# Kernel optimization log

Measured on AMD Instinct MI355X. Metric: run time of the kernel, lower is better.

The kernel has to match this reference:

```python
import jax, jax.numpy as jnp
import numpy as np

B, N, D = 8, 9856, 256
HEADS = 8
WH, WW = 7, 11
HID = 512  # int(D * 2.0)
EPS = 1e-5


def layernorm(x, g, b):
    mu = jnp.mean(x, axis=-1, keepdims=True)
    var = jnp.mean(jnp.square(x - mu), axis=-1, keepdims=True)
    return (x - mu) * jax.lax.rsqrt(var + EPS) * g + b


def setup_inputs() -> dict:
    key = jax.random.key(0)
    ks = jax.random.split(key, 6)
    s = lambda k, shape: (jax.random.normal(k, shape, jnp.float32) * 0.02)
    return {
        "x": jax.random.normal(ks[0], (B, N, D), jnp.float32),
        "norm1_g": jnp.ones((D,), jnp.float32),
        "norm1_b": jnp.zeros((D,), jnp.float32),
        "in_proj_w": s(ks[1], (3 * D, D)),
        "in_proj_b": jnp.zeros((3 * D,), jnp.float32),
        "out_w": s(ks[2], (D, D)),
        "out_b": jnp.zeros((D,), jnp.float32),
        "norm2_g": jnp.ones((D,), jnp.float32),
        "norm2_b": jnp.zeros((D,), jnp.float32),
        "fc1_w": s(ks[3], (HID, D)),
        "fc1_b": jnp.zeros((HID,), jnp.float32),
        "fc2_w": s(ks[4], (D, HID)),
        "fc2_b": jnp.zeros((D,), jnp.float32),
        "h": 56,
        "w": 176,
    }


def reference(x, norm1_g, norm1_b, in_proj_w, in_proj_b, out_w, out_b,
              norm2_g, norm2_b, fc1_w, fc1_b, fc2_w, fc2_b, h, w):
    Bx, Nx, Dx = x.shape
    n_h, n_w = h // WH, w // WW  # chosen dims divide evenly -> pad_h = pad_w = 0
    hd = Dx // HEADS
    L = WH * WW  # 77 tokens per window

    res = x
    xn = layernorm(x, norm1_g, norm1_b)

    # window partition: (B, h*w, D) -> (B*n_h*n_w, wh*ww, D)
    win = xn.reshape(Bx, n_h, WH, n_w, WW, Dx)
    win = win.transpose(0, 1, 3, 2, 4, 5).reshape(-1, L, Dx)

    # MultiheadAttention (batch_first) on each window independently
    qkv = win @ in_proj_w.T + in_proj_b          # (NW, L, 3D)
    q, k, v = jnp.split(qkv, 3, axis=-1)
    NW = win.shape[0]
    q = q.reshape(NW, L, HEADS, hd).transpose(0, 2, 1, 3)
    k = k.reshape(NW, L, HEADS, hd).transpose(0, 2, 1, 3)
    v = v.reshape(NW, L, HEADS, hd).transpose(0, 2, 1, 3)
    scores = jnp.einsum("nhld,nhmd->nhlm", q, k) / jnp.sqrt(jnp.float32(hd))
    attn = jax.nn.softmax(scores, axis=-1)
    o = jnp.einsum("nhlm,nhmd->nhld", attn, v)   # (NW, H, L, hd)
    o = o.transpose(0, 2, 1, 3).reshape(NW, L, Dx)
    o = o @ out_w.T + out_b

    # window reverse: (B*n_h*n_w, wh*ww, D) -> (B, h*w, D)
    o = o.reshape(Bx, n_h, n_w, WH, WW, Dx)
    o = o.transpose(0, 1, 3, 2, 4, 5).reshape(Bx, Nx, Dx)

    x = res + o
    res = x
    xn2 = layernorm(x, norm2_g, norm2_b)
    hmid = jax.nn.gelu(xn2 @ fc1_w.T + fc1_b, approximate=False)
    mlp = hmid @ fc2_w.T + fc2_b
    return res + mlp
```

## Files before the change

### kernel.cpp

```cpp
#include <hip/hip_runtime.h>
#include <hip/hip_bf16.h>

typedef unsigned short u16;
typedef unsigned int   u32;

typedef __bf16 bf16x8 __attribute__((ext_vector_type(8)));
typedef float  f32x4  __attribute__((ext_vector_type(4)));

__device__ __forceinline__ u16 f2bf(float f) {
  u32 u = __float_as_uint(f);
  u += 0x7fffu + ((u >> 16) & 1u);
  return (u16)(u >> 16);
}
__device__ __forceinline__ u32 pack2(float a, float b) {
  return (u32)f2bf(a) | ((u32)f2bf(b) << 16);
}
__device__ __forceinline__ void gld16(const void* g, void* l) {
  __builtin_amdgcn_global_load_lds(
      (const __attribute__((address_space(1))) unsigned int*)g,
      (__attribute__((address_space(3))) unsigned int*)l, 16, 0, 0);
}

#define TOK_M   78848
#define DIM     256
#define NWIN    1024
#define WINL    77

__global__ __launch_bounds__(256)
void cvt_w(const float* __restrict__ w0, const float* __restrict__ w1,
           const float* __restrict__ w2, const float* __restrict__ w3,
           u16* __restrict__ out)
{
  const int i = (blockIdx.x * 256 + threadIdx.x) * 4;
  const float* src; int off;
  if      (i < 196608) { src = w0; off = i; }
  else if (i < 262144) { src = w1; off = i - 196608; }
  else if (i < 393216) { src = w2; off = i - 262144; }
  else                 { src = w3; off = i - 393216; }
  float4 v = *(const float4*)(src + off);
  uint2 o; o.x = pack2(v.x, v.y); o.y = pack2(v.z, v.w);
  *(uint2*)(out + i) = o;
}

template<bool PERM>
__global__ __launch_bounds__(256)
void ln_k(const float* __restrict__ X, const float* __restrict__ g,
          const float* __restrict__ bta, u16* __restrict__ Y)
{
  const int tid  = threadIdx.x;
  const int tok  = blockIdx.x * 4 + (tid >> 6);
  const int lane = tid & 63;
  float4 v = *(const float4*)(X + (size_t)tok * DIM + lane * 4);
  float s = v.x + v.y + v.z + v.w;
#pragma unroll
  for (int off = 32; off; off >>= 1) s += __shfl_xor(s, off);
  const float mu = s * (1.f / 256.f);
  const float dx = v.x - mu, dy = v.y - mu, dz = v.z - mu, dw = v.w - mu;
  float q = dx * dx + dy * dy + dz * dz + dw * dw;
#pragma unroll
  for (int off = 32; off; off >>= 1) q += __shfl_xor(q, off);
  const float rstd = rsqrtf(q * (1.f / 256.f) + 1e-5f);
  float4 gg = *(const float4*)(g + lane * 4);
  float4 bb = *(const float4*)(bta + lane * 4);
  const float y0 = dx * rstd * gg.x + bb.x;
  const float y1 = dy * rstd * gg.y + bb.y;
  const float y2 = dz * rstd * gg.z + bb.z;
  const float y3 = dw * rstd * gg.w + bb.w;
  size_t dest = (size_t)tok;
  if (PERM) {
    const int b  = tok / 9856, n = tok - b * 9856;
    const int y  = n / 176,  xc = n - y * 176;
    const int ih = y / 7,    rr = y - ih * 7;
    const int iw = xc / 11,  cc = xc - iw * 11;
    dest = (size_t)(((b * 8 + ih) * 16 + iw)) * 77 + rr * 11 + cc;
  }
  uint2 o;
  o.x = pack2(y0, y1);
  o.y = pack2(y2, y3);
  *(uint2*)(Y + dest * DIM + lane * 4) = o;
}

template<int EPI, int OBF>
__global__ __launch_bounds__(256, 3)
void gemm_mfma(const u16* __restrict__ A, const u16* __restrict__ W,
               const float* __restrict__ bias, const float* res,
               void* Cout, int N, int K)
{
  __shared__ u16 As[4096];
  __shared__ u16 Bs[4096];

  const int tid  = threadIdx.x;
  const int wave = tid >> 6, lane = tid & 63;
  const int wy = wave >> 1, wx = wave & 1;
  const int quad = lane >> 4, l16 = lane & 15;
  const int m0 = blockIdx.x * 128;
  const int n0 = blockIdx.y * 128;

  const int s0 = tid, s1 = tid + 256;
  const int r0 = s0 >> 2, r1 = s1 >> 2;
  const int kb0 = (s0 & 3) ^ (r0 & 3);
  const int kb1 = (s1 & 3) ^ (r1 & 3);
  const u16* Ag0 = A + (size_t)(m0 + r0) * K + kb0 * 8;
  const u16* Ag1 = A + (size_t)(m0 + r1) * K + kb1 * 8;
  const u16* Bg0 = W + (size_t)(n0 + r0) * K + kb0 * 8;
  const u16* Bg1 = W + (size_t)(n0 + r1) * K + kb1 * 8;

  const int kbs = quad ^ (l16 & 3);
  const u16* Ar = &As[(wy * 64 + l16) * 32 + kbs * 8];
  const u16* Br = &Bs[(wx * 64 + l16) * 32 + kbs * 8];

  f32x4 acc[4][4];
#pragma unroll
  for (int i = 0; i < 4; ++i)
#pragma unroll
    for (int j = 0; j < 4; ++j) {
      f32x4 z = {0.f, 0.f, 0.f, 0.f};
      acc[i][j] = z;
    }

  for (int kt = 0; kt < K; kt += 32) {
    gld16(Ag0 + kt, &As[s0 * 8]);
    gld16(Ag1 + kt, &As[s1 * 8]);
    gld16(Bg0 + kt, &Bs[s0 * 8]);
    gld16(Bg1 + kt, &Bs[s1 * 8]);
    __syncthreads();
    bf16x8 af[4], bv[4];
#pragma unroll
    for (int i = 0; i < 4; ++i) {
      af[i] = *(const bf16x8*)(Ar + i * 16 * 32);
      bv[i] = *(const bf16x8*)(Br + i * 16 * 32);
    }
#pragma unroll
    for (int mi = 0; mi < 4; ++mi)
#pragma unroll
      for (int ni = 0; ni < 4; ++ni)
        acc[mi][ni] = __builtin_amdgcn_mfma_f32_16x16x32_bf16(
            af[mi], bv[ni], acc[mi][ni], 0, 0, 0);
    __syncthreads();
  }

  const int gr0 = m0 + wy * 64 + quad * 4;
  const int gc0 = n0 + wx * 64 + l16;
#pragma unroll
  for (int ni = 0; ni < 4; ++ni) {
    const int gc = gc0 + ni * 16;
    const float bvs = bias[gc];
#pragma unroll
    for (int mi = 0; mi < 4; ++mi) {
      const int gr = gr0 + mi * 16;
      f32x4 a = acc[mi][ni];
#pragma unroll
      for (int e = 0; e < 4; ++e) {
        float v = a[e] + bvs;
        const size_t idx = (size_t)(gr + e) * N + gc;
        if (EPI == 1) v += res[idx];
        else if (EPI == 2) v = 0.5f * v * (1.f + erff(v * 0.70710678118654752f));
        if (OBF) ((u16*)Cout)[idx] = f2bf(v);
        else     ((float*)Cout)[idx] = v;
      }
    }
  }
}

#define PSTR 104
__global__ __launch_bounds__(128)
void attn_mfma(const u16* __restrict__ qkv, u16* __restrict__ onat)
{
  __shared__ __bf16 Pb[2][80 * PSTR];

  const int tid  = threadIdx.x;
  const int wave = tid >> 6, lane = tid & 63;
  const int quad = lane >> 4, l16 = lane & 15;
  const int pair = blockIdx.x * 2 + wave;
  const int nw   = pair >> 3, head = pair & 7;
  const size_t base = (size_t)nw * 77 * 768;
  const int hoff = head * 32;
  __bf16* P = Pb[wave];

  {
    uint4 z = {0, 0, 0, 0};
    for (int r = lane; r < 80; r += 64) {
      *(uint4*)(P + r * PSTR + 80) = z;
      *(uint4*)(P + r * PSTR + 88) = z;
    }
  }

  bf16x8 qf[5], kf[5];
  const u16* qp = qkv + base + hoff + quad * 8;
#pragma unroll
  for (int mi = 0; mi < 5; ++mi) {
    const size_t row = (size_t)(l16 + 16 * mi) * 768;
    qf[mi] = *(const bf16x8*)(qp + row);
    kf[mi] = *(const bf16x8*)(qp + row + 256);
  }

  f32x4 s[5][5];
#pragma unroll
  for (int mi = 0; mi < 5; ++mi)
#pragma unroll
    for (int ni = 0; ni < 5; ++ni) {
      f32x4 z = {0.f, 0.f, 0.f, 0.f};
      s[mi][ni] = z;
    }
#pragma unroll
  for (int mi = 0; mi < 5; ++mi)
#pragma unroll
    for (int ni = 0; ni < 5; ++ni)
      s[mi][ni] = __builtin_amdgcn_mfma_f32_16x16x32_bf16(
          qf[mi], kf[ni], s[mi][ni], 0, 0, 0);

  bf16x8 vf[3][2];
  {
    const __bf16* vbb = (const __bf16*)(qkv + base + 512 + hoff + l16);
#pragma unroll
    for (int ks = 0; ks < 3; ++ks)
#pragma unroll
      for (int ni = 0; ni < 2; ++ni)
#pragma unroll
        for (int jj = 0; jj < 8; ++jj) {
          const int k = ks * 32 + quad * 8 + jj;
          vf[ks][ni][jj] = (k < 77) ? vbb[(size_t)k * 768 + 16 * ni] : (__bf16)0.f;
        }
  }

  if (l16 >= 13) {
#pragma unroll
    for (int mi = 0; mi < 5; ++mi)
#pragma unroll
      for (int e = 0; e < 4; ++e) s[mi][4][e] = -1e30f;
  }

  const float c = 0.17677669529663687f * 1.4426950408889634f;
  float inv[5][4];
#pragma unroll
  for (int mi = 0; mi < 5; ++mi)
#pragma unroll
    for (int e = 0; e < 4; ++e) {
      float mx = s[mi][0][e];
#pragma unroll
      for (int ni = 1; ni < 5; ++ni) mx = fmaxf(mx, s[mi][ni][e]);
#pragma unroll
      for (int off = 1; off < 16; off <<= 1) mx = fmaxf(mx, __shfl_xor(mx, off));
      float sum = 0.f;
#pragma unroll
      for (int ni = 0; ni < 5; ++ni) {
        const float ev = exp2f((s[mi][ni][e] - mx) * c);
        s[mi][ni][e] = ev;
        sum += ev;
      }
#pragma unroll
      for (int off = 1; off < 16; off <<= 1) sum += __shfl_xor(sum, off);
      inv[mi][e] = 1.f / sum;
    }

#pragma unroll
  for (int mi = 0; mi < 5; ++mi)
#pragma unroll
    for (int e = 0; e < 4; ++e) {
      const int m = quad * 4 + e + 16 * mi;
#pragma unroll
      for (int ni = 0; ni < 5; ++ni)
        P[m * PSTR + l16 + 16 * ni] = (__bf16)(s[mi][ni][e] * inv[mi][e]);
    }

  f32x4 o[5][2];
#pragma unroll
  for (int mi = 0; mi < 5; ++mi)
#pragma unroll
    for (int ni = 0; ni < 2; ++ni) {
      f32x4 z = {0.f, 0.f, 0.f, 0.f};
      o[mi][ni] = z;
    }
#pragma unroll
  for (int ks = 0; ks < 3; ++ks)
#pragma unroll
    for (int mi = 0; mi < 5; ++mi) {
      const bf16x8 af = *(const bf16x8*)(P + (l16 + 16 * mi) * PSTR + ks * 32 + quad * 8);
#pragma unroll
      for (int ni = 0; ni < 2; ++ni)
        o[mi][ni] = __builtin_amdgcn_mfma_f32_16x16x32_bf16(
            af, vf[ks][ni], o[mi][ni], 0, 0, 0);
    }

  const int b  = nw >> 7;
  const int ih = (nw >> 4) & 7;
  const int iw = nw & 15;
#pragma unroll
  for (int mi = 0; mi < 5; ++mi)
#pragma unroll
    for (int e = 0; e < 4; ++e) {
      const int t = quad * 4 + e + 16 * mi;
      if (t < 77) {
        const int rr = t / 11, cc = t - rr * 11;
        const int y = ih * 7 + rr, xc = iw * 11 + cc;
        const size_t nat = (size_t)b * 9856 + (size_t)y * 176 + xc;
        u16* dst = onat + nat * DIM + hoff + l16;
        dst[0]  = f2bf(o[mi][0][e]);
        dst[16] = f2bf(o[mi][1][e]);
      }
    }
}

extern "C" void kernel_launch(void* const* d_in, const int* in_sizes, int n_in,
                              void* d_out, int out_size, void* d_ws, size_t ws_size,
                              hipStream_t stream)
{
  (void)in_sizes; (void)n_in; (void)out_size; (void)ws_size;
  const float* x    = (const float*)d_in[0];
  const float* g1   = (const float*)d_in[1];
  const float* b1   = (const float*)d_in[2];
  const float* wqkv = (const float*)d_in[3];
  const float* bqkv = (const float*)d_in[4];
  const float* wout = (const float*)d_in[5];
  const float* bout = (const float*)d_in[6];
  const float* g2   = (const float*)d_in[7];
  const float* b2   = (const float*)d_in[8];
  const float* w1   = (const float*)d_in[9];
  const float* bf1  = (const float*)d_in[10];
  const float* w2   = (const float*)d_in[11];
  const float* bf2  = (const float*)d_in[12];

  char* ws = (char*)d_ws;
  u16*   qkv  = (u16*)(ws);
  u16*   xn   = (u16*)(ws + 121110528);
  u16*   onat = (u16*)(ws + 161480704);
  u16*   wb   = (u16*)(ws + 201850880);
  u16*   wqkv_b = wb;
  u16*   wout_b = wb + 196608;
  u16*   w1_b   = wb + 262144;
  u16*   w2_b   = wb + 393216;
  float* x2   = (float*)d_out;

  cvt_w<<<512, 256, 0, stream>>>(wqkv, wout, w1, w2, wb);
  ln_k<true><<<19712, 256, 0, stream>>>(x, g1, b1, xn);
  gemm_mfma<0, 1><<<dim3(616, 6), 256, 0, stream>>>(xn, wqkv_b, bqkv, nullptr, qkv, 768, 256);
  attn_mfma<<<4096, 128, 0, stream>>>(qkv, onat);
  gemm_mfma<1, 0><<<dim3(616, 2), 256, 0, stream>>>(onat, wout_b, bout, x, x2, 256, 256);
  ln_k<false><<<19712, 256, 0, stream>>>(x2, g2, b2, xn);
  gemm_mfma<2, 1><<<dim3(616, 4), 256, 0, stream>>>(xn, w1_b, bf1, nullptr, qkv, 512, 256);
  gemm_mfma<1, 0><<<dim3(616, 2), 256, 0, stream>>>(qkv, w2_b, bf2, x2, x2, 256, 512);
}
```

Measured before the change: 603.1 us.

## Replace LDS-staged GEMM with direct-register GEMM looping over all N tiles

The shared-memory tiled GEMM with global_load_lds and per-k barriers is replaced by a kernel that loads A and W fragments straight from global memory into registers. Each block keeps its 128-row A slice in registers for K=256 and loops over every N tile itself, so A is read once per block and the kernel has no LDS traffic or syncthreads. The cost is much higher register pressure (32 bf16x8 A fragments plus accumulators), lower occupancy (launch bounds 2), and uncoalesced per-lane W loads that rely on the cache. The K=512 case reloads A fragments from global memory on each N tile.

```diff
diff --git a/kernel.cpp b/kernel.cpp
--- a/kernel.cpp
+++ b/kernel.cpp
@@ -14,11 +14,6 @@
 }
 __device__ __forceinline__ u32 pack2(float a, float b) {
   return (u32)f2bf(a) | ((u32)f2bf(b) << 16);
-}
-__device__ __forceinline__ void gld16(const void* g, void* l) {
-  __builtin_amdgcn_global_load_lds(
-      (const __attribute__((address_space(1))) unsigned int*)g,
-      (__attribute__((address_space(3))) unsigned int*)l, 16, 0, 0);
 }
 
 #define TOK_M   78848
@@ -80,83 +75,86 @@
   *(uint2*)(Y + dest * DIM + lane * 4) = o;
 }
 
-template<int EPI, int OBF>
-__global__ __launch_bounds__(256, 3)
-void gemm_mfma(const u16* __restrict__ A, const u16* __restrict__ W,
-               const float* __restrict__ bias, const float* res,
-               void* Cout, int N, int K)
-{
-  __shared__ u16 As[4096];
-  __shared__ u16 Bs[4096];
-
+template<int NT, int KS, int EPI, int OBF>
+__global__ __launch_bounds__(256, 2)
+void gemm_direct(const u16* __restrict__ A, const u16* __restrict__ W,
+                 const float* __restrict__ bias, const float* __restrict__ res,
+                 void* __restrict__ Cout)
+{
+  constexpr int K = KS * 32;
+  constexpr int N = NT * 128;
   const int tid  = threadIdx.x;
   const int wave = tid >> 6, lane = tid & 63;
   const int wy = wave >> 1, wx = wave & 1;
   const int quad = lane >> 4, l16 = lane & 15;
   const int m0 = blockIdx.x * 128;
-  const int n0 = blockIdx.y * 128;
-
-  const int s0 = tid, s1 = tid + 256;
-  const int r0 = s0 >> 2, r1 = s1 >> 2;
-  const int kb0 = (s0 & 3) ^ (r0 & 3);
-  const int kb1 = (s1 & 3) ^ (r1 & 3);
-  const u16* Ag0 = A + (size_t)(m0 + r0) * K + kb0 * 8;
-  const u16* Ag1 = A + (size_t)(m0 + r1) * K + kb1 * 8;
-  const u16* Bg0 = W + (size_t)(n0 + r0) * K + kb0 * 8;
-  const u16* Bg1 = W + (size_t)(n0 + r1) * K + kb1 * 8;
-
-  const int kbs = quad ^ (l16 & 3);
-  const u16* Ar = &As[(wy * 64 + l16) * 32 + kbs * 8];
-  const u16* Br = &Bs[(wx * 64 + l16) * 32 + kbs * 8];
-
-  f32x4 acc[4][4];
-#pragma unroll
-  for (int i = 0; i < 4; ++i)
-#pragma unroll
-    for (int j = 0; j < 4; ++j) {
-      f32x4 z = {0.f, 0.f, 0.f, 0.f};
-      acc[i][j] = z;
-    }
-
-  for (int kt = 0; kt < K; kt += 32) {
-    gld16(Ag0 + kt, &As[s0 * 8]);
-    gld16(Ag1 + kt, &As[s1 * 8]);
-    gld16(Bg0 + kt, &Bs[s0 * 8]);
-    gld16(Bg1 + kt, &Bs[s1 * 8]);
-    __syncthreads();
-    bf16x8 af[4], bv[4];
-#pragma unroll
-    for (int i = 0; i < 4; ++i) {
-      af[i] = *(const bf16x8*)(Ar + i * 16 * 32);
-      bv[i] = *(const bf16x8*)(Br + i * 16 * 32);
-    }
+
+  const u16* Ap = A + (size_t)(m0 + wy * 64 + l16) * K + quad * 8;
+  const u16* Wp = W + (size_t)(wx * 64 + l16) * K + quad * 8;
+
+  bf16x8 af[4][8];
+  if constexpr (KS <= 8) {
 #pragma unroll
     for (int mi = 0; mi < 4; ++mi)
 #pragma unroll
+      for (int ks = 0; ks < KS; ++ks)
+        af[mi][ks] = *(const bf16x8*)(Ap + (size_t)mi * 16 * K + ks * 32);
+  }
+
+#pragma unroll
+  for (int nt = 0; nt < NT; ++nt) {
+    const u16* Wn = Wp + (size_t)nt * 128 * K;
+    f32x4 acc[4][4];
+#pragma unroll
+    for (int i = 0; i < 4; ++i)
+#pragma unroll
+      for (int j = 0; j < 4; ++j) {
+        f32x4 z = {0.f, 0.f, 0.f, 0.f};
+        acc[i][j] = z;
+      }
+
+#pragma unroll
+    for (int ks = 0; ks < KS; ++ks) {
+      bf16x8 bv[4];
+#pragma unroll
       for (int ni = 0; ni < 4; ++ni)
-        acc[mi][ni] = __builtin_amdgcn_mfma_f32_16x16x32_bf16(
-            af[mi], bv[ni], acc[mi][ni], 0, 0, 0);
-    __syncthreads();
-  }
-
-  const int gr0 = m0 + wy * 64 + quad * 4;
-  const int gc0 = n0 + wx * 64 + l16;
-#pragma unroll
-  for (int ni = 0; ni < 4; ++ni) {
-    const int gc = gc0 + ni * 16;
-    const float bvs = bias[gc];
-#pragma unroll
-    for (int mi = 0; mi < 4; ++mi) {
-      const int gr = gr0 + mi * 16;
-      f32x4 a = acc[mi][ni];
-#pragma unroll
-      for (int e = 0; e < 4; ++e) {
-        float v = a[e] + bvs;
-        const size_t idx = (size_t)(gr + e) * N + gc;
-        if (EPI == 1) v += res[idx];
-        else if (EPI == 2) v = 0.5f * v * (1.f + erff(v * 0.70710678118654752f));
-        if (OBF) ((u16*)Cout)[idx] = f2bf(v);
-        else     ((float*)Cout)[idx] = v;
+        bv[ni] = *(const bf16x8*)(Wn + (size_t)ni * 16 * K + ks * 32);
+      bf16x8 av[4];
+      if constexpr (KS <= 8) {
+#pragma unroll
+        for (int mi = 0; mi < 4; ++mi) av[mi] = af[mi][ks];
+      } else {
+#pragma unroll
+        for (int mi = 0; mi < 4; ++mi)
+          av[mi] = *(const bf16x8*)(Ap + (size_t)mi * 16 * K + ks * 32);
+      }
+#pragma unroll
+      for (int mi = 0; mi < 4; ++mi)
+#pragma unroll
+        for (int ni = 0; ni < 4; ++ni)
+          acc[mi][ni] = __builtin_amdgcn_mfma_f32_16x16x32_bf16(
+              av[mi], bv[ni], acc[mi][ni], 0, 0, 0);
+    }
+
+    const int gr0 = m0 + wy * 64 + quad * 4;
+    const int gc0 = nt * 128 + wx * 64 + l16;
+#pragma unroll
+    for (int ni = 0; ni < 4; ++ni) {
+      const int gc = gc0 + ni * 16;
+      const float bvs = bias[gc];
+#pragma unroll
+      for (int mi = 0; mi < 4; ++mi) {
+        const int gr = gr0 + mi * 16;
+        f32x4 a = acc[mi][ni];
+#pragma unroll
+        for (int e = 0; e < 4; ++e) {
+          float v = a[e] + bvs;
+          const size_t idx = (size_t)(gr + e) * N + gc;
+          if (EPI == 1) v += res[idx];
+          else if (EPI == 2) v = 0.5f * v * (1.f + erff(v * 0.70710678118654752f));
+          if (OBF) ((u16*)Cout)[idx] = f2bf(v);
+          else     ((float*)Cout)[idx] = v;
+        }
       }
     }
   }
@@ -275,11 +273,11 @@
   for (int ks = 0; ks < 3; ++ks)
 #pragma unroll
     for (int mi = 0; mi < 5; ++mi) {
-      const bf16x8 af = *(const bf16x8*)(P + (l16 + 16 * mi) * PSTR + ks * 32 + quad * 8);
+      const bf16x8 afr = *(const bf16x8*)(P + (l16 + 16 * mi) * PSTR + ks * 32 + quad * 8);
 #pragma unroll
       for (int ni = 0; ni < 2; ++ni)
         o[mi][ni] = __builtin_amdgcn_mfma_f32_16x16x32_bf16(
-            af, vf[ks][ni], o[mi][ni], 0, 0, 0);
+            afr, vf[ks][ni], o[mi][ni], 0, 0, 0);
     }
 
   const int b  = nw >> 7;
@@ -333,10 +331,10 @@
 
   cvt_w<<<512, 256, 0, stream>>>(wqkv, wout, w1, w2, wb);
   ln_k<true><<<19712, 256, 0, stream>>>(x, g1, b1, xn);
-  gemm_mfma<0, 1><<<dim3(616, 6), 256, 0, stream>>>(xn, wqkv_b, bqkv, nullptr, qkv, 768, 256);
+  gemm_direct<6, 8, 0, 1><<<616, 256, 0, stream>>>(xn, wqkv_b, bqkv, nullptr, qkv);
   attn_mfma<<<4096, 128, 0, stream>>>(qkv, onat);
-  gemm_mfma<1, 0><<<dim3(616, 2), 256, 0, stream>>>(onat, wout_b, bout, x, x2, 256, 256);
+  gemm_direct<2, 8, 1, 0><<<616, 256, 0, stream>>>(onat, wout_b, bout, x, x2);
   ln_k<false><<<19712, 256, 0, stream>>>(x2, g2, b2, xn);
-  gemm_mfma<2, 1><<<dim3(616, 4), 256, 0, stream>>>(xn, w1_b, bf1, nullptr, qkv, 512, 256);
-  gemm_mfma<1, 0><<<dim3(616, 2), 256, 0, stream>>>(qkv, w2_b, bf2, x2, x2, 256, 512);
-}
+  gemm_direct<4, 8, 2, 1><<<616, 256, 0, stream>>>(xn, w1_b, bf1, nullptr, qkv);
+  gemm_direct<2, 16, 1, 0><<<616, 256, 0, stream>>>(qkv, w2_b, bf2, x2, x2);
+}
```

Result: slower. 892.9 us (+48.0%).
